# Optimization experiments

Measured on AMD Instinct MI355X. Metric: run time of the kernel, lower is better.

The kernel has to match this reference:

```python
import jax, jax.numpy as jnp
import numpy as np
import math

D_MODEL = 128
B, H, S, D = 4, 16, 2048, 128

def setup_inputs() -> dict:
    key = jax.random.key(0)
    kq, kk, kv, km = jax.random.split(key, 4)
    q = jax.random.normal(kq, (B, H, S, D), dtype=jnp.float32)
    k = jax.random.normal(kk, (B, H, S, D), dtype=jnp.float32)
    v = jax.random.normal(kv, (B, H, S, D), dtype=jnp.float32)
    mask = jax.random.randint(km, (1, 1, S, S), 0, 2, dtype=jnp.int32)
    return {"q": q, "k": k, "v": v, "mask": mask}

def reference(q, k, v, mask):
    scale = 1.0 / math.sqrt(D_MODEL)
    # [B,H,S,S] score matrix (faithful to the unfused original)
    scores = jnp.einsum('bhsd,bhtd->bhst', q, k) * scale
    neg = jnp.finfo(scores.dtype).min
    scores = jnp.where(mask == 0, neg, scores)
    attn = jax.nn.softmax(scores, axis=-1)
    return jnp.einsum('bhst,bhtd->bhsd', attn, v)
```

## Files before the change

### kernel.cpp

```cpp
#include <hip/hip_runtime.h>
#include <hip/hip_bf16.h>
#include <stdint.h>

#define S_LEN 2048
#define D_HEAD 128
#define TILE_T 64
#define QTILE 256
#define NTHREADS 512
#define N_TILES (S_LEN / TILE_T)
#define NBH 64

typedef __attribute__((ext_vector_type(8))) __bf16 bf16x8;
typedef __attribute__((ext_vector_type(4))) float f32x4;
typedef __attribute__((ext_vector_type(4))) float fvec4;
typedef __attribute__((ext_vector_type(2))) float fvec2;

__device__ __forceinline__ __bf16 to_bf16_rne(float f) {
    unsigned u = __builtin_bit_cast(unsigned, f);
    u += 0x7FFFu + ((u >> 16) & 1u);
    unsigned short h = (unsigned short)(u >> 16);
    return __builtin_bit_cast(__bf16, h);
}

__device__ __forceinline__ int swz(int row, int elem) {
    return elem ^ (((row ^ (row >> 3)) & 7) << 3);
}

__global__ void pack_mask_kernel(const int* __restrict__ mask,
                                 unsigned long long* __restrict__ bits)
{
    const int i = blockIdx.x * 256 + threadIdx.x;
    const unsigned long long b = __ballot(mask[i] != 0);
    if ((threadIdx.x & 63) == 0) bits[i >> 6] = b;
}

__global__ __launch_bounds__(NTHREADS, 2)
void sdpa_flash_kernel(const float* __restrict__ q,
                       const float* __restrict__ k,
                       const float* __restrict__ v,
                       const unsigned long long* __restrict__ mbits,
                       float* __restrict__ out)
{
    __shared__ __align__(16) __bf16 Ks[TILE_T * D_HEAD];
    __shared__ __align__(16) __bf16 Vs[D_HEAD * TILE_T];
    __shared__ __align__(16) __bf16 Ps[QTILE * TILE_T];

    const int tid  = threadIdx.x;
    const int wave = tid >> 6;
    const int lane = tid & 63;
    const int quad = lane >> 4;
    const int lc   = lane & 15;

    const int q0 = blockIdx.x * QTILE;
    const int bh = blockIdx.y;

    const float* qbh = q + (size_t)bh * S_LEN * D_HEAD;
    const float* kbh = k + (size_t)bh * S_LEN * D_HEAD;
    const float* vbh = v + (size_t)bh * S_LEN * D_HEAD;

    bf16x8 qf[2][4];
    #pragma unroll
    for (int mt = 0; mt < 2; ++mt) {
        const float* qrow = qbh + (size_t)(q0 + wave * 32 + mt * 16 + lc) * D_HEAD + quad * 8;
        #pragma unroll
        for (int kc = 0; kc < 4; ++kc) {
            fvec4 a = *(const fvec4*)(qrow + kc * 32);
            fvec4 b = *(const fvec4*)(qrow + kc * 32 + 4);
            bf16x8 f;
            #pragma unroll
            for (int j = 0; j < 4; ++j) {
                f[j]     = to_bf16_rne(a[j]);
                f[4 + j] = to_bf16_rne(b[j]);
            }
            qf[mt][kc] = f;
        }
    }

    f32x4 o_acc[2][8];
    #pragma unroll
    for (int mt = 0; mt < 2; ++mt)
        #pragma unroll
        for (int i = 0; i < 8; ++i) o_acc[mt][i] = (f32x4){0.f, 0.f, 0.f, 0.f};
    float l_lane[2][4];
    #pragma unroll
    for (int mt = 0; mt < 2; ++mt)
        #pragma unroll
        for (int r = 0; r < 4; ++r) l_lane[mt][r] = 0.f;

    const float scale = 0.08838834764831845f;

    for (int kt = 0; kt < N_TILES; ++kt) {
        __syncthreads();

        {
            const float* kg = kbh + (size_t)kt * TILE_T * D_HEAD;
            #pragma unroll
            for (int i = 0; i < 2; ++i) {
                const int idx = tid + i * NTHREADS;
                const int r   = idx >> 4;
                const int c8  = (idx & 15) << 3;
                fvec4 a = *(const fvec4*)(kg + r * D_HEAD + c8);
                fvec4 b = *(const fvec4*)(kg + r * D_HEAD + c8 + 4);
                bf16x8 kw;
                #pragma unroll
                for (int j = 0; j < 4; ++j) {
                    kw[j]     = to_bf16_rne(a[j]);
                    kw[4 + j] = to_bf16_rne(b[j]);
                }
                *(bf16x8*)(&Ks[swz(r, (r << 7) + c8)]) = kw;
            }
        }

        {
            const float* vg = vbh + (size_t)kt * TILE_T * D_HEAD;
            const int t0 = wave << 3;
            const int d0 = (tid & 63) << 1;
            fvec2 w2[8];
            #pragma unroll
            for (int j = 0; j < 8; ++j)
                w2[j] = *(const fvec2*)(vg + (size_t)(t0 + j) * D_HEAD + d0);
            #pragma unroll
            for (int e = 0; e < 2; ++e) {
                uint32_t rp[4];
                #pragma unroll
                for (int p = 0; p < 4; ++p) {
                    const unsigned ha = (unsigned)__builtin_bit_cast(unsigned short, to_bf16_rne(w2[2 * p][e]));
                    const unsigned hb = (unsigned)__builtin_bit_cast(unsigned short, to_bf16_rne(w2[2 * p + 1][e]));
                    rp[p] = ha | (hb << 16);
                }
                const int d = d0 + e;
                *(uint4*)(&Vs[swz(d, (d << 6) + t0)]) = *(const uint4*)rp;
            }
        }

        __syncthreads();

        f32x4 s_acc[2][4];
        #pragma unroll
        for (int mt = 0; mt < 2; ++mt)
            #pragma unroll
            for (int nt = 0; nt < 4; ++nt) s_acc[mt][nt] = (f32x4){0.f, 0.f, 0.f, 0.f};
        #pragma unroll
        for (int nt = 0; nt < 4; ++nt)
            #pragma unroll
            for (int kc = 0; kc < 4; ++kc) {
                const int rk = nt * 16 + lc;
                bf16x8 kf = *(const bf16x8*)(&Ks[swz(rk, (rk << 7) + kc * 32 + quad * 8)]);
                s_acc[0][nt] = __builtin_amdgcn_mfma_f32_16x16x32_bf16(qf[0][kc], kf, s_acc[0][nt], 0, 0, 0);
                s_acc[1][nt] = __builtin_amdgcn_mfma_f32_16x16x32_bf16(qf[1][kc], kf, s_acc[1][nt], 0, 0, 0);
            }

        #pragma unroll
        for (int mt = 0; mt < 2; ++mt)
            #pragma unroll
            for (int r = 0; r < 4; ++r) {
                const unsigned long long mk =
                    mbits[(size_t)(q0 + wave * 32 + mt * 16 + quad * 4 + r) * N_TILES + kt];
                const uint32_t lo = (uint32_t)mk;
                const uint32_t hi = (uint32_t)(mk >> 32);
                const int prow = wave * 32 + mt * 16 + quad * 4 + r;
                #pragma unroll
                for (int nt = 0; nt < 4; ++nt) {
                    const uint32_t h   = (nt & 2) ? hi : lo;
                    const uint32_t bit = (h >> ((nt & 1) * 16 + lc)) & 1u;
                    const float sv = s_acc[mt][nt][r] * scale;
                    const float ev = bit ? __expf(sv) : 0.0f;
                    const __bf16 eb = to_bf16_rne(ev);
                    l_lane[mt][r] += (float)eb;
                    Ps[swz(prow, (prow << 6) + nt * 16 + lc)] = eb;
                }
            }


        #pragma unroll
        for (int c = 0; c < 2; ++c) {
            const int ra0 = wave * 32 + lc;
            const int ra1 = wave * 32 + 16 + lc;
            bf16x8 af0 = *(const bf16x8*)(&Ps[swz(ra0, (ra0 << 6) + c * 32 + quad * 8)]);
            bf16x8 af1 = *(const bf16x8*)(&Ps[swz(ra1, (ra1 << 6) + c * 32 + quad * 8)]);
            #pragma unroll
            for (int dt = 0; dt < 8; ++dt) {
                const int rv = dt * 16 + lc;
                bf16x8 vf = *(const bf16x8*)(&Vs[swz(rv, (rv << 6) + c * 32 + quad * 8)]);
                o_acc[0][dt] = __builtin_amdgcn_mfma_f32_16x16x32_bf16(af0, vf, o_acc[0][dt], 0, 0, 0);
                o_acc[1][dt] = __builtin_amdgcn_mfma_f32_16x16x32_bf16(af1, vf, o_acc[1][dt], 0, 0, 0);
            }
        }
    }

    #pragma unroll
    for (int mt = 0; mt < 2; ++mt)
        #pragma unroll
        for (int r = 0; r < 4; ++r) {
            float s = l_lane[mt][r];
            #pragma unroll
            for (int off = 1; off < 16; off <<= 1)
                s += __shfl_xor(s, off, 64);
            l_lane[mt][r] = s;
        }

    float* obh = out + (size_t)bh * S_LEN * D_HEAD;
    #pragma unroll
    for (int mt = 0; mt < 2; ++mt)
        #pragma unroll
        for (int r = 0; r < 4; ++r) {
            float inv = 1.0f / l_lane[mt][r];
            const size_t row = (size_t)(q0 + wave * 32 + mt * 16 + quad * 4 + r) * D_HEAD;
            #pragma unroll
            for (int dt = 0; dt < 8; ++dt)
                obh[row + dt * 16 + lc] = o_acc[mt][dt][r] * inv;
        }
}

extern "C" void kernel_launch(void* const* d_in, const int* in_sizes, int n_in,
                              void* d_out, int out_size, void* d_ws, size_t ws_size,
                              hipStream_t stream)
{
    const float* q    = (const float*)d_in[0];
    const float* k    = (const float*)d_in[1];
    const float* v    = (const float*)d_in[2];
    const int*   mask = (const int*)d_in[3];
    float* out = (float*)d_out;

    unsigned long long* mbits = (unsigned long long*)d_ws;

    pack_mask_kernel<<<dim3(S_LEN * S_LEN / 256), 256, 0, stream>>>(mask, mbits);
    sdpa_flash_kernel<<<dim3(S_LEN / QTILE, NBH), NTHREADS, 0, stream>>>(q, k, v, mbits, out);
}
```

Measured before the change: 527.1 us.

## Prefetch next K/V tile into registers, fold scale into Q, use exp2

Global loads of the next K and V tile go into registers right after the barrier, so their latency overlaps with the QK and PV MFMA work of the current tile. The softmax scale and log2(e) are folded into Q before its bf16 conversion, so the inner loop can call a raw exp2 and drop a multiply per score. s_setprio wraps the MFMA sections to favour matrix issue across waves. The extra prefetch registers may raise register pressure at 2 blocks per CU, and pre-scaling Q slightly changes bf16 rounding.

```diff
diff --git a/kernel.cpp b/kernel.cpp
--- a/kernel.cpp
+++ b/kernel.cpp
@@ -14,6 +14,12 @@
 typedef __attribute__((ext_vector_type(4))) float f32x4;
 typedef __attribute__((ext_vector_type(4))) float fvec4;
 typedef __attribute__((ext_vector_type(2))) float fvec2;
+
+#if __has_builtin(__builtin_amdgcn_exp2f)
+#define EXP2(x) __builtin_amdgcn_exp2f(x)
+#else
+#define EXP2(x) exp2f(x)
+#endif
 
 __device__ __forceinline__ __bf16 to_bf16_rne(float f) {
     unsigned u = __builtin_bit_cast(unsigned, f);
@@ -58,6 +64,7 @@
     const float* kbh = k + (size_t)bh * S_LEN * D_HEAD;
     const float* vbh = v + (size_t)bh * S_LEN * D_HEAD;
 
+    const float qscale = 0.08838834764831845f * 1.4426950408889634f;
     bf16x8 qf[2][4];
     #pragma unroll
     for (int mt = 0; mt < 2; ++mt) {
@@ -69,8 +76,8 @@
             bf16x8 f;
             #pragma unroll
             for (int j = 0; j < 4; ++j) {
-                f[j]     = to_bf16_rne(a[j]);
-                f[4 + j] = to_bf16_rne(b[j]);
+                f[j]     = to_bf16_rne(a[j] * qscale);
+                f[4 + j] = to_bf16_rne(b[j] * qscale);
             }
             qf[mt][kc] = f;
         }
@@ -87,59 +94,68 @@
         #pragma unroll
         for (int r = 0; r < 4; ++r) l_lane[mt][r] = 0.f;
 
-    const float scale = 0.08838834764831845f;
+    const int vt0 = wave << 3;
+    const int vd0 = (tid & 63) << 1;
+    fvec4 kr[2][2];
+    fvec2 vr[8];
+    auto load_kv = [&](int kt_) {
+        const float* kg = kbh + (size_t)kt_ * TILE_T * D_HEAD;
+        const float* vg = vbh + (size_t)kt_ * TILE_T * D_HEAD;
+        #pragma unroll
+        for (int i = 0; i < 2; ++i) {
+            const int idx = tid + i * NTHREADS;
+            const int r   = idx >> 4;
+            const int c8  = (idx & 15) << 3;
+            kr[i][0] = *(const fvec4*)(kg + r * D_HEAD + c8);
+            kr[i][1] = *(const fvec4*)(kg + r * D_HEAD + c8 + 4);
+        }
+        #pragma unroll
+        for (int j = 0; j < 8; ++j)
+            vr[j] = *(const fvec2*)(vg + (size_t)(vt0 + j) * D_HEAD + vd0);
+    };
+
+    load_kv(0);
 
     for (int kt = 0; kt < N_TILES; ++kt) {
         __syncthreads();
 
-        {
-            const float* kg = kbh + (size_t)kt * TILE_T * D_HEAD;
-            #pragma unroll
-            for (int i = 0; i < 2; ++i) {
-                const int idx = tid + i * NTHREADS;
-                const int r   = idx >> 4;
-                const int c8  = (idx & 15) << 3;
-                fvec4 a = *(const fvec4*)(kg + r * D_HEAD + c8);
-                fvec4 b = *(const fvec4*)(kg + r * D_HEAD + c8 + 4);
-                bf16x8 kw;
-                #pragma unroll
-                for (int j = 0; j < 4; ++j) {
-                    kw[j]     = to_bf16_rne(a[j]);
-                    kw[4 + j] = to_bf16_rne(b[j]);
-                }
-                *(bf16x8*)(&Ks[swz(r, (r << 7) + c8)]) = kw;
-            }
-        }
-
-        {
-            const float* vg = vbh + (size_t)kt * TILE_T * D_HEAD;
-            const int t0 = wave << 3;
-            const int d0 = (tid & 63) << 1;
-            fvec2 w2[8];
-            #pragma unroll
-            for (int j = 0; j < 8; ++j)
-                w2[j] = *(const fvec2*)(vg + (size_t)(t0 + j) * D_HEAD + d0);
-            #pragma unroll
-            for (int e = 0; e < 2; ++e) {
-                uint32_t rp[4];
-                #pragma unroll
-                for (int p = 0; p < 4; ++p) {
-                    const unsigned ha = (unsigned)__builtin_bit_cast(unsigned short, to_bf16_rne(w2[2 * p][e]));
-                    const unsigned hb = (unsigned)__builtin_bit_cast(unsigned short, to_bf16_rne(w2[2 * p + 1][e]));
-                    rp[p] = ha | (hb << 16);
-                }
-                const int d = d0 + e;
-                *(uint4*)(&Vs[swz(d, (d << 6) + t0)]) = *(const uint4*)rp;
-            }
+        #pragma unroll
+        for (int i = 0; i < 2; ++i) {
+            const int idx = tid + i * NTHREADS;
+            const int r   = idx >> 4;
+            const int c8  = (idx & 15) << 3;
+            bf16x8 kw;
+            #pragma unroll
+            for (int j = 0; j < 4; ++j) {
+                kw[j]     = to_bf16_rne(kr[i][0][j]);
+                kw[4 + j] = to_bf16_rne(kr[i][1][j]);
+            }
+            *(bf16x8*)(&Ks[swz(r, (r << 7) + c8)]) = kw;
+        }
+
+        #pragma unroll
+        for (int e = 0; e < 2; ++e) {
+            uint32_t rp[4];
+            #pragma unroll
+            for (int p = 0; p < 4; ++p) {
+                const unsigned ha = (unsigned)__builtin_bit_cast(unsigned short, to_bf16_rne(vr[2 * p][e]));
+                const unsigned hb = (unsigned)__builtin_bit_cast(unsigned short, to_bf16_rne(vr[2 * p + 1][e]));
+                rp[p] = ha | (hb << 16);
+            }
+            const int d = vd0 + e;
+            *(uint4*)(&Vs[swz(d, (d << 6) + vt0)]) = *(const uint4*)rp;
         }
 
         __syncthreads();
 
+        if (kt + 1 < N_TILES) load_kv(kt + 1);
+
         f32x4 s_acc[2][4];
         #pragma unroll
         for (int mt = 0; mt < 2; ++mt)
             #pragma unroll
             for (int nt = 0; nt < 4; ++nt) s_acc[mt][nt] = (f32x4){0.f, 0.f, 0.f, 0.f};
+        __builtin_amdgcn_s_setprio(1);
         #pragma unroll
         for (int nt = 0; nt < 4; ++nt)
             #pragma unroll
@@ -149,6 +165,7 @@
                 s_acc[0][nt] = __builtin_amdgcn_mfma_f32_16x16x32_bf16(qf[0][kc], kf, s_acc[0][nt], 0, 0, 0);
                 s_acc[1][nt] = __builtin_amdgcn_mfma_f32_16x16x32_bf16(qf[1][kc], kf, s_acc[1][nt], 0, 0, 0);
             }
+        __builtin_amdgcn_s_setprio(0);
 
         #pragma unroll
         for (int mt = 0; mt < 2; ++mt)
@@ -163,8 +180,7 @@
                 for (int nt = 0; nt < 4; ++nt) {
                     const uint32_t h   = (nt & 2) ? hi : lo;
                     const uint32_t bit = (h >> ((nt & 1) * 16 + lc)) & 1u;
-                    const float sv = s_acc[mt][nt][r] * scale;
-                    const float ev = bit ? __expf(sv) : 0.0f;
+                    const float ev = bit ? EXP2(s_acc[mt][nt][r]) : 0.0f;
                     const __bf16 eb = to_bf16_rne(ev);
                     l_lane[mt][r] += (float)eb;
                     Ps[swz(prow, (prow << 6) + nt * 16 + lc)] = eb;
@@ -172,6 +188,7 @@
             }
 
 
+        __builtin_amdgcn_s_setprio(1);
         #pragma unroll
         for (int c = 0; c < 2; ++c) {
             const int ra0 = wave * 32 + lc;
@@ -186,6 +203,7 @@
                 o_acc[1][dt] = __builtin_amdgcn_mfma_f32_16x16x32_bf16(af1, vf, o_acc[1][dt], 0, 0, 0);
             }
         }
+        __builtin_amdgcn_s_setprio(0);
     }
 
     #pragma unroll
```

New measurement: 481.2 us. -8.7%, faster.
